# Performance work log

Measured on AMD Instinct MI355X. Metric: run time of the kernel, lower is better.

The kernel has to match this reference:

```python
import jax, jax.numpy as jnp
import numpy as np

N, L, H, E, V, PAD = 128, 64, 512, 512, 32000, 0


def setup_inputs() -> dict:
    key = jax.random.key(0)
    ks = jax.random.split(key, 8)
    s_in = 1.0 / np.sqrt(E)
    s_sani = 1.0 / np.sqrt(2 * H)
    s_out = 1.0 / np.sqrt(H)
    labels = jax.random.randint(ks[0], (N, L), 0, V)
    emb_table = jax.random.normal(ks[1], (V, E), jnp.float32) * 0.02
    emb_table = emb_table.at[PAD].set(0.0)  # padding_idx row is zero-initialized
    W_in = jax.random.uniform(ks[2], (H, E), jnp.float32, -s_in, s_in)
    b_in = jax.random.uniform(ks[3], (H,), jnp.float32, -s_in, s_in)
    W_sani = jax.random.uniform(ks[4], (H, 2 * H), jnp.float32, -s_sani, s_sani)
    b_sani = jax.random.uniform(ks[5], (H,), jnp.float32, -s_sani, s_sani)
    W_out = jax.random.uniform(ks[6], (E, H), jnp.float32, -s_out, s_out)
    b_out = jax.random.uniform(ks[7], (E,), jnp.float32, -s_out, s_out)
    return dict(labels=labels, emb_table=emb_table, W_in=W_in, b_in=b_in,
                W_sani=W_sani, b_sani=b_sani, W_out=W_out, b_out=b_out)


def reference(labels, emb_table, W_in, b_in, W_sani, b_sani, W_out, b_out):
    n, l = labels.shape
    emb = emb_table[labels]                                   # [N,L,E]
    x = jnp.einsum('nle,he->nlh', emb, W_in) + b_in           # [N,L,H] input conversion
    h_dim = W_in.shape[0]

    def step(states, sc):
        s, h0 = sc                                            # h0: [N,H]
        def body(li, carry):
            h, st = carry
            prev = st[li]                                     # hiddenStateLast[li]
            new_h = jnp.concatenate([prev, h], axis=-1) @ W_sani.T + b_sani
            take = li < s                                     # triangular mask
            return (jnp.where(take, new_h, h),
                    st.at[li].set(jnp.where(take, h, prev)))
        h, states = jax.lax.fori_loop(0, l, body, (h0, states))
        states = states.at[s].set(h)                          # hiddenStateLast[s] = h
        return states, h                                      # outputStates[s] = h

    states0 = jnp.zeros((l, n, h_dim), x.dtype)
    _, outs = jax.lax.scan(step, states0, (jnp.arange(l), jnp.swapaxes(x, 0, 1)))
    # torch: pt.concat(outputStates, dim=0) -> [L*N, H], outputLayer, reshape(N,L,E)
    y = outs.reshape(l * n, h_dim) @ W_out.T + b_out
    y = y.reshape(n, l, E)  # faithful to the original (sequence-major) reshape
    # CrossEntropyLoss with float (probability) targets: classes along dim 1 (L)
    logp = jax.nn.log_softmax(y, axis=1)
    loss = -(emb * logp).sum(axis=1).mean()
    return loss
```

## Files before the change

### kernel.cpp

```cpp
#include <hip/hip_runtime.h>
#include <hip/hip_bf16.h>

typedef __attribute__((ext_vector_type(8))) short short8;
typedef __attribute__((ext_vector_type(4))) float floatx4;

#define NB 128
#define LS 64
#define HD 512
#define ED 512
#define NH 65536
#define LDA 72
#define LDC 136
#define LDCF 132

#define OFF_WIN    0ull
#define OFF_WOUT   524288ull
#define OFF_XT     1048576ull
#define OFF_LVL0   9437184ull
#define OFF_LVL1   17825792ull
#define OFF_OUTS   26214400ull
#define OFF_PHA    34603008ull
#define OFF_PLA    37224448ull
#define OFF_PHB    39845888ull
#define OFF_PLB    42467328ull
#define OFF_BCAT   45088768ull
#define OFF_BETA   52428800ull
#define OFF_PART   52436992ull
#define OFF_WSLO   52437504ull
#define OFF_Y      OFF_LVL0

static __device__ __forceinline__ unsigned short f2b(float f) {
  unsigned u = __float_as_uint(f);
  u += 0x7fffu + ((u >> 16) & 1u);
  return (unsigned short)(u >> 16);
}
static __device__ __forceinline__ float b2f(unsigned short h) {
  return __uint_as_float(((unsigned)h) << 16);
}

static __device__ __forceinline__ void gl_lds16(const unsigned short* g, unsigned short* l) {
  __builtin_amdgcn_global_load_lds(
      (const __attribute__((address_space(1))) void*)g,
      (__attribute__((address_space(3))) void*)l, 16, 0, 0);
}

static __device__ __forceinline__ uint4 cvt8hi(const float* s) {
  floatx4 f0 = *(const floatx4*)s;
  floatx4 f1 = *(const floatx4*)(s + 4);
  float f[8] = {f0.x, f0.y, f0.z, f0.w, f1.x, f1.y, f1.z, f1.w};
  unsigned short b[8];
#pragma unroll
  for (int k = 0; k < 8; ++k) b[k] = f2b(f[k]);
  uint4 u;
  u.x = b[0] | ((unsigned)b[1] << 16); u.y = b[2] | ((unsigned)b[3] << 16);
  u.z = b[4] | ((unsigned)b[5] << 16); u.w = b[6] | ((unsigned)b[7] << 16);
  return u;
}

__device__ __forceinline__ void gemm_core24(const unsigned short* As, const unsigned short* Bs,
                                            floatx4 acc[2][4], int wm, int wn, int lane) {
  const int rb = lane & 15;
  const int kg = (lane >> 4) * 8;
#pragma unroll
  for (int kk = 0; kk < 64; kk += 32) {
    short8 a[2], b[4];
#pragma unroll
    for (int i = 0; i < 2; ++i)
      a[i] = *(const short8*)&As[(wm * 32 + i * 16 + rb) * LDA + kk + kg];
#pragma unroll
    for (int j = 0; j < 4; ++j)
      b[j] = *(const short8*)&Bs[(wn * 64 + j * 16 + rb) * LDA + kk + kg];
#pragma unroll
    for (int i = 0; i < 2; ++i)
#pragma unroll
      for (int j = 0; j < 4; ++j)
        acc[i][j] = __builtin_amdgcn_mfma_f32_16x16x32_bf16(a[i], b[j], acc[i][j], 0, 0, 0);
  }
}

__device__ __forceinline__ void gemm_core64s(const unsigned short* As, const unsigned short* Bs,
                                             floatx4 acc[2][4], int wm, int wn, int lane) {
  const int rb = lane & 15;
  const int kg = (lane >> 4) * 8;
  const int xv = (rb & 7) * 8;
#pragma unroll
  for (int kk = 0; kk < 64; kk += 32) {
    const int co = (kk + kg) ^ xv;
    short8 a[2], b[4];
#pragma unroll
    for (int i = 0; i < 2; ++i)
      a[i] = *(const short8*)&As[(wm * 32 + i * 16 + rb) * 64 + co];
#pragma unroll
    for (int j = 0; j < 4; ++j)
      b[j] = *(const short8*)&Bs[(wn * 64 + j * 16 + rb) * 64 + co];
#pragma unroll
    for (int i = 0; i < 2; ++i)
#pragma unroll
      for (int j = 0; j < 4; ++j)
        acc[i][j] = __builtin_amdgcn_mfma_f32_16x16x32_bf16(a[i], b[j], acc[i][j], 0, 0, 0);
  }
}

__device__ __forceinline__ void stageA_emb(unsigned short* As, const float* table,
                                           const int* labels, int m0, int k0, int tid) {
  int r = tid >> 3, kc = (tid & 7) * 8;
#pragma unroll
  for (int p = 0; p < 2; ++p) {
    int row = r + p * 32;
    const float* s = table + (size_t)labels[m0 + row] * ED + k0 + kc;
    *(uint4*)&As[row * LDA + kc] = cvt8hi(s);
  }
}

__device__ __forceinline__ void stageB(unsigned short* Bs, const unsigned short* src, int ldB, int tid) {
  int r = tid >> 3, kc = (tid & 7) * 8;
#pragma unroll
  for (int p = 0; p < 4; ++p)
    *(uint4*)&Bs[(r + p * 32) * LDA + kc] = *(const uint4*)(src + (size_t)(r + p * 32) * ldB + kc);
}

__global__ __launch_bounds__(256) void k_gemm_emb(const float* __restrict__ table,
                                                  const int* __restrict__ labels,
                                                  const unsigned short* __restrict__ Wb,
                                                  const float* __restrict__ bias,
                                                  unsigned short* __restrict__ xt,
                                                  unsigned short* __restrict__ outs) {
  __shared__ unsigned short As[64 * LDA];
  __shared__ unsigned short Bs[128 * LDA];
  int tid = threadIdx.x;
  int mtile = blockIdx.x >> 2, ntile = blockIdx.x & 3;
  int m0 = mtile * 64, n0 = ntile * 128;
  int lane = tid & 63, wave = tid >> 6, wm = wave >> 1, wn = wave & 1;
  floatx4 acc[2][4] = {};
  for (int k0 = 0; k0 < 512; k0 += 64) {
    stageA_emb(As, table, labels, m0, k0, tid);
    stageB(Bs, Wb + (size_t)n0 * 512 + k0, 512, tid);
    __syncthreads();
    gemm_core24(As, Bs, acc, wm, wn, lane);
    __syncthreads();
  }
  int rb = lane & 15, rg = (lane >> 4) * 4;
#pragma unroll
  for (int i = 0; i < 2; ++i)
#pragma unroll
    for (int j = 0; j < 4; ++j) {
      int col = n0 + wn * 64 + j * 16 + rb;
      float bv = bias[col];
#pragma unroll
      for (int reg = 0; reg < 4; ++reg) {
        int m = m0 + wm * 32 + i * 16 + rg + reg;
        int n = m >> 6, l = m & 63;
        unsigned short v = f2b(acc[i][j][reg] + bv);
        xt[((size_t)l * NB + n) * HD + col] = v;
        if (l == 0) outs[(size_t)n * HD + col] = v;
      }
    }
}

__global__ __launch_bounds__(256) void k_cvtw(const float* __restrict__ Win,
                                              const float* __restrict__ Wsani,
                                              const float* __restrict__ Wout,
                                              unsigned short* __restrict__ dWin,
                                              unsigned short* __restrict__ dBcat1,
                                              unsigned short* __restrict__ dWsLo,
                                              unsigned short* __restrict__ dWout) {
  int i = blockIdx.x * 256 + threadIdx.x;
  if (i < 65536 || i >= 196608) {
    const float* src = (i < 65536) ? Win : Wout;
    unsigned short* dst = (i < 65536) ? dWin : dWout;
    int off = (i < 65536) ? i : i - 196608;
    floatx4 v = *(const floatx4*)(src + (size_t)off * 4);
    uint2 u;
    u.x = (unsigned)f2b(v.x) | ((unsigned)f2b(v.y) << 16);
    u.y = (unsigned)f2b(v.z) | ((unsigned)f2b(v.w) << 16);
    *(uint2*)(dst + (size_t)off * 4) = u;
  } else {
    int off = i - 65536;
    floatx4 v = *(const floatx4*)(Wsani + (size_t)off * 4);
    float f[4] = {v.x, v.y, v.z, v.w};
    unsigned short hb[4], lb[4];
#pragma unroll
    for (int k = 0; k < 4; ++k) {
      hb[k] = f2b(f[k]);
      lb[k] = f2b(f[k] - b2f(hb[k]));
    }
    uint2 h, l;
    h.x = hb[0] | ((unsigned)hb[1] << 16); h.y = hb[2] | ((unsigned)hb[3] << 16);
    l.x = lb[0] | ((unsigned)lb[1] << 16); l.y = lb[2] | ((unsigned)lb[3] << 16);
    *(uint2*)(dBcat1 + (size_t)off * 4) = h;
    *(uint2*)(dWsLo + (size_t)off * 4) = l;
  }
}

__global__ __launch_bounds__(256) void k_trW(const float* __restrict__ Ws,
                                             unsigned short* __restrict__ Phi,
                                             unsigned short* __restrict__ Plo) {
  __shared__ float t[64][65];
  int mat = blockIdx.x >> 6, tile = blockIdx.x & 63;
  int a0 = (tile >> 3) * 64, b0 = (tile & 7) * 64;
  int coloff = (mat == 0) ? 512 : 0;
  for (int pp = 0; pp < 16; ++pp) {
    int idx = pp * 256 + threadIdx.x, rr = idx >> 6, cc = idx & 63;
    t[rr][cc] = Ws[(size_t)(b0 + rr) * 1024 + coloff + a0 + cc];
  }
  __syncthreads();
  for (int pp = 0; pp < 16; ++pp) {
    int idx = pp * 256 + threadIdx.x, rr = idx >> 6, cc = idx & 63;
    float f = t[cc][rr];
    unsigned short hi = f2b(f);
    size_t o = (size_t)mat * 262144 + (size_t)(a0 + rr) * 512 + b0 + cc;
    Phi[o] = hi;
    Plo[o] = f2b(f - b2f(hi));
  }
}

__global__ __launch_bounds__(256) void k_coef(const unsigned short* __restrict__ Phi,
                                              const unsigned short* __restrict__ Plo,
                                              unsigned short* __restrict__ PhiOut,
                                              unsigned short* __restrict__ PloOut,
                                              const unsigned short* __restrict__ WsHi,
                                              const unsigned short* __restrict__ WsLo,
                                              int m) {
  __shared__ unsigned short lds[24576];
  unsigned short* const A0 = lds;
  unsigned short* const A1 = lds + 4096;
  unsigned short* const B0 = lds + 8192;
  unsigned short* const B1 = lds + 16384;
  const int tid = threadIdx.x;
  const int j = blockIdx.x >> 5, tile = blockIdx.x & 31;
  const int k0r = (tile >> 2) * 64, n0 = (tile & 3) * 128;
  const int lane = tid & 63, wave = tid >> 6, wm = wave >> 1, wn = wave & 1;
  const int rr_ = tid >> 3;
  const int kcs = (((tid & 7) ^ ((tid >> 3) & 7))) * 8;
  const int t_first = (j <= m) ? 0 : 1;
  const int nterms = ((j <= m) ? 1 : 0) + ((j >= 1) ? 1 : 0);
  const int nsteps = nterms * 24;

  floatx4 acc[2][4] = {};

#define STAGE_C(Ab, Bb, u)                                                           \
  { int term_ = t_first + (((u) >= 24) ? 1 : 0);                                     \
    int v_ = ((u) >> 3) % 3;                                                         \
    int t0_ = ((u) & 7) * 64;                                                        \
    const unsigned short* As_ = ((v_ == 2) ? Plo : Phi)                              \
        + (size_t)(term_ ? (j - 1) : j) * 262144 + (size_t)k0r * 512 + t0_;          \
    const unsigned short* Bs_ = ((v_ == 1) ? WsLo : WsHi)                            \
        + (size_t)n0 * 1024 + (term_ ? 0 : 512) + t0_;                               \
    unsigned short* lA = (Ab) + (tid >> 6) * 512;                                    \
    unsigned short* lB = (Bb) + (tid >> 6) * 512;                                    \
    gl_lds16(As_ + (size_t)rr_ * 512 + kcs, lA);                                     \
    gl_lds16(As_ + (size_t)(rr_ + 32) * 512 + kcs, lA + 2048);                       \
    gl_lds16(Bs_ + (size_t)rr_ * 1024 + kcs, lB);                                    \
    gl_lds16(Bs_ + (size_t)(rr_ + 32) * 1024 + kcs, lB + 2048);                      \
    gl_lds16(Bs_ + (size_t)(rr_ + 64) * 1024 + kcs, lB + 4096);                      \
    gl_lds16(Bs_ + (size_t)(rr_ + 96) * 1024 + kcs, lB + 6144); }

  STAGE_C(A0, B0, 0)
  __syncthreads();
  for (int u = 0; u < nsteps; u += 2) {
    if (u + 1 < nsteps) STAGE_C(A1, B1, u + 1)
    gemm_core64s(A0, B0, acc, wm, wn, lane);
    __syncthreads();
    if (u + 2 < nsteps) STAGE_C(A0, B0, u + 2)
    gemm_core64s(A1, B1, acc, wm, wn, lane);
    __syncthreads();
  }
#undef STAGE_C

  const int rb = lane & 15, rg = (lane >> 4) * 4;
#pragma unroll
  for (int i = 0; i < 2; ++i)
#pragma unroll
    for (int jj = 0; jj < 4; ++jj) {
      int col = n0 + wn * 64 + jj * 16 + rb;
#pragma unroll
      for (int reg = 0; reg < 4; ++reg) {
        int row = wm * 32 + i * 16 + rg + reg;
        float f = acc[i][jj][reg];
        unsigned short hi = f2b(f);
        size_t o = (size_t)j * 262144 + (size_t)(k0r + row) * 512 + col;
        PhiOut[o] = hi;
        PloOut[o] = f2b(f - b2f(hi));
      }
    }
}

__global__ __launch_bounds__(256) void k_trB(const unsigned short* __restrict__ Phi,
                                             unsigned short* __restrict__ Bout,
                                             int r) {
  __shared__ unsigned short t[64][68];
  int q = blockIdx.x >> 6, tile = blockIdx.x & 63;
  int t0 = (tile >> 3) * 64, i0 = (tile & 7) * 64;
  const unsigned short* P = Phi + (size_t)(r - q) * 262144;
  int ldB = (r + 1) * 512;
  for (int pp = 0; pp < 16; ++pp) {
    int idx = pp * 256 + threadIdx.x, rr = idx >> 6, cc = idx & 63;
    t[rr][cc] = P[(size_t)(t0 + rr) * 512 + i0 + cc];
  }
  __syncthreads();
  for (int pp = 0; pp < 16; ++pp) {
    int idx = pp * 256 + threadIdx.x, rr = idx >> 6, cc = idx & 63;
    Bout[(size_t)(i0 + rr) * ldB + q * 512 + t0 + cc] = t[cc][rr];
  }
}

__global__ __launch_bounds__(64) void k_bias_step(const float* __restrict__ Ws,
                                                  const float* __restrict__ b,
                                                  const float* __restrict__ bprev,
                                                  float* __restrict__ bout) {
  int i = blockIdx.x, t = threadIdx.x;
  float p = 0.f;
  for (int k = t; k < 512; k += 64)
    p += (Ws[(size_t)i * 1024 + k] + Ws[(size_t)i * 1024 + 512 + k]) * bprev[k];
#pragma unroll
  for (int off = 32; off > 0; off >>= 1) p += __shfl_down(p, off, 64);
  if (t == 0) bout[i] = p + b[i];
}

__global__ __launch_bounds__(256) void k_step(const unsigned short* __restrict__ src,
                                              unsigned short* __restrict__ dst,
                                              unsigned short* __restrict__ outs,
                                              const unsigned short* __restrict__ Bcat,
                                              const float* __restrict__ beta,
                                              int L_prev, int m, int nmain, int g) {
  __shared__ unsigned short lds[24576];
  unsigned short* const A0 = lds;
  unsigned short* const A1 = lds + 4096;
  unsigned short* const B0 = lds + 8192;
  unsigned short* const B1 = lds + 16384;
  const int tid = threadIdx.x, bid = blockIdx.x;
  const int mainWG = 32 * g;
  int r, s, nb0, n0;
  if (bid < mainWG) {
    const int xcd = bid & 7, w = bid >> 3;
    const int sgrp = xcd >> 1, ngrp = xcd & 1;
    const int s_rel = sgrp * g + (w >> 2);
    if (s_rel >= nmain) return;
    const int sub2 = w & 3;
    nb0 = (sub2 >> 1) * 64;
    n0 = (ngrp * 2 + (sub2 & 1)) * 128;
    r = m; s = L_prev + m + s_rel;
  } else {
    const int db = bid - mainWG;
    r = 1 + (db >> 3);
    const int sub = db & 7;
    nb0 = (sub >> 2) * 64; n0 = (sub & 3) * 128;
    s = L_prev + r;
  }
  const int ldB = (r + 1) * 512;
  const unsigned short* Bp = Bcat + (size_t)262144 * (((r - 1) * (r + 2)) >> 1);
  const unsigned short* abase = src + (size_t)(s - r) * NH + (size_t)nb0 * HD;
  const float* bet = beta + (size_t)(r - 1) * 512;
  const int nk = (r + 1) * 8;
  const int lane = tid & 63, wave = tid >> 6, wm = wave >> 1, wn = wave & 1;
  const int rr_ = tid >> 3;
  const int kcs = (((tid & 7) ^ ((tid >> 3) & 7))) * 8;

  floatx4 acc[2][4] = {};

#define STAGE(Ab, Bb, kcol)                                                          \
  { int q_ = (kcol) >> 9, ac_ = (kcol) & 511;                                        \
    const unsigned short* a0_ = abase + (size_t)q_ * NH + ac_;                       \
    unsigned short* lA = (Ab) + (tid >> 6) * 512;                                    \
    unsigned short* lB = (Bb) + (tid >> 6) * 512;                                    \
    gl_lds16(a0_ + (size_t)rr_ * HD + kcs, lA);                                      \
    gl_lds16(a0_ + (size_t)(rr_ + 32) * HD + kcs, lA + 2048);                        \
    gl_lds16(Bp + (size_t)(n0 + rr_) * ldB + (kcol) + kcs, lB);                      \
    gl_lds16(Bp + (size_t)(n0 + rr_ + 32) * ldB + (kcol) + kcs, lB + 2048);          \
    gl_lds16(Bp + (size_t)(n0 + rr_ + 64) * ldB + (kcol) + kcs, lB + 4096);          \
    gl_lds16(Bp + (size_t)(n0 + rr_ + 96) * ldB + (kcol) + kcs, lB + 6144); }

  STAGE(A0, B0, 0)
  __syncthreads();
  for (int k = 0; k < nk; k += 2) {
    if (k + 1 < nk) STAGE(A1, B1, (k + 1) * 64)
    gemm_core64s(A0, B0, acc, wm, wn, lane);
    __syncthreads();
    if (k + 2 < nk) STAGE(A0, B0, (k + 2) * 64)
    gemm_core64s(A1, B1, acc, wm, wn, lane);
    __syncthreads();
  }
#undef STAGE

  unsigned short* Ct = lds;
  const int rbc = lane & 15, rg = (lane >> 4) * 4;
#pragma unroll
  for (int i = 0; i < 2; ++i)
#pragma unroll
    for (int j = 0; j < 4; ++j) {
      int col = wn * 64 + j * 16 + rbc;
      float bv = bet[n0 + col];
#pragma unroll
      for (int reg = 0; reg < 4; ++reg) {
        int row = wm * 32 + i * 16 + rg + reg;
        Ct[row * LDC + col] = f2b(acc[i][j][reg] + bv);
      }
    }
  __syncthreads();
  const bool wdst = (r == m);
  const bool wout = (r < m) || (s == L_prev + m);
  unsigned short* d1 = dst  + (size_t)s * NH + (size_t)nb0 * HD + n0;
  unsigned short* d2 = outs + (size_t)s * NH + (size_t)nb0 * HD + n0;
  const int lrow = tid >> 4, lcol = (tid & 15) * 8;
#pragma unroll
  for (int sweep = 0; sweep < 4; ++sweep) {
    int row = sweep * 16 + lrow;
    uint4 v = *(const uint4*)&Ct[row * LDC + lcol];
    if (wdst) *(uint4*)(d1 + (size_t)row * HD + lcol) = v;
    if (wout) *(uint4*)(d2 + (size_t)row * HD + lcol) = v;
  }
}

__global__ __launch_bounds__(256) void k_gemm_out(const unsigned short* __restrict__ outs,
                                                  const unsigned short* __restrict__ Wb,
                                                  const float* __restrict__ bias,
                                                  float* __restrict__ Y) {
  __shared__ unsigned short lds[24576];
  unsigned short* const A0 = lds;
  unsigned short* const A1 = lds + 4096;
  unsigned short* const B0 = lds + 8192;
  unsigned short* const B1 = lds + 16384;
  const int tid = threadIdx.x;
  const int mtile = blockIdx.x >> 2, ntile = blockIdx.x & 3;
  const int m0 = mtile * 64, n0 = ntile * 128;
  const int lane = tid & 63, wave = tid >> 6, wm = wave >> 1, wn = wave & 1;
  const int rr_ = tid >> 3;
  const int kcs = (((tid & 7) ^ ((tid >> 3) & 7))) * 8;
  const unsigned short* abase = outs + (size_t)m0 * 512;
  const unsigned short* Bp = Wb + (size_t)n0 * 512;

  floatx4 acc[2][4] = {};

#define STAGE_O(Ab, Bb, kcol)                                                        \
  { unsigned short* lA = (Ab) + (tid >> 6) * 512;                                    \
    unsigned short* lB = (Bb) + (tid >> 6) * 512;                                    \
    gl_lds16(abase + (size_t)rr_ * 512 + (kcol) + kcs, lA);                          \
    gl_lds16(abase + (size_t)(rr_ + 32) * 512 + (kcol) + kcs, lA + 2048);            \
    gl_lds16(Bp + (size_t)rr_ * 512 + (kcol) + kcs, lB);                             \
    gl_lds16(Bp + (size_t)(rr_ + 32) * 512 + (kcol) + kcs, lB + 2048);               \
    gl_lds16(Bp + (size_t)(rr_ + 64) * 512 + (kcol) + kcs, lB + 4096);               \
    gl_lds16(Bp + (size_t)(rr_ + 96) * 512 + (kcol) + kcs, lB + 6144); }

  STAGE_O(A0, B0, 0)
  __syncthreads();
  for (int k = 0; k < 8; k += 2) {
    if (k + 1 < 8) STAGE_O(A1, B1, (k + 1) * 64)
    gemm_core64s(A0, B0, acc, wm, wn, lane);
    __syncthreads();
    if (k + 2 < 8) STAGE_O(A0, B0, (k + 2) * 64)
    gemm_core64s(A1, B1, acc, wm, wn, lane);
    __syncthreads();
  }
#undef STAGE_O

  float* Ctf = (float*)lds;
  const int rbc = lane & 15, rg = (lane >> 4) * 4;
#pragma unroll
  for (int i = 0; i < 2; ++i)
#pragma unroll
    for (int j = 0; j < 4; ++j) {
      int col = wn * 64 + j * 16 + rbc;
      float bv = bias[n0 + col];
#pragma unroll
      for (int reg = 0; reg < 4; ++reg) {
        int row = wm * 32 + i * 16 + rg + reg;
        Ctf[row * LDCF + col] = acc[i][j][reg] + bv;
      }
    }
  __syncthreads();
  const int lrow = tid >> 5, lc = (tid & 31) * 4;
#pragma unroll
  for (int sweep = 0; sweep < 8; ++sweep) {
    int row = sweep * 8 + lrow;
    uint4 v = *(const uint4*)&Ctf[row * LDCF + lc];
    *(uint4*)&Y[(size_t)(m0 + row) * 512 + n0 + lc] = v;
  }
}

__global__ void k_copy(const uint4* __restrict__ src, uint4* __restrict__ dst, int n) {
  int i = blockIdx.x * blockDim.x + threadIdx.x;
  if (i < n) dst[i] = src[i];
}

__global__ __launch_bounds__(256) void k_loss(const float* __restrict__ Y,
                                              const float* __restrict__ table,
                                              const int* __restrict__ labels,
                                              float* __restrict__ partials) {
  int n = blockIdx.x, tid = threadIdx.x;
  float total = 0.f;
#pragma unroll
  for (int e2 = 0; e2 < 2; ++e2) {
    int e = e2 * 256 + tid;
    float mx = -1e30f;
    for (int l = 0; l < 64; ++l)
      mx = fmaxf(mx, Y[(size_t)(n * 64 + l) * 512 + e]);
    float se = 0.f;
    for (int l = 0; l < 64; ++l)
      se += expf(Y[(size_t)(n * 64 + l) * 512 + e] - mx);
    float lse = mx + logf(se);
    for (int l = 0; l < 64; ++l) {
      float embv = table[(size_t)labels[n * 64 + l] * ED + e];
      total += embv * (Y[(size_t)(n * 64 + l) * 512 + e] - lse);
    }
  }
  __shared__ float red[256];
  red[tid] = total;
  __syncthreads();
  for (int s2 = 128; s2 > 0; s2 >>= 1) {
    if (tid < s2) red[tid] += red[tid + s2];
    __syncthreads();
  }
  if (tid == 0) partials[n] = red[0];
}

__global__ void k_final(const float* __restrict__ partials, float* __restrict__ out) {
  if (threadIdx.x == 0) {
    double s = 0.0;
    for (int i = 0; i < 128; ++i) s += (double)partials[i];
    out[0] = (float)(-s / 65536.0);
  }
}

extern "C" void kernel_launch(void* const* d_in, const int* in_sizes, int n_in,
                              void* d_out, int out_size, void* d_ws, size_t ws_size,
                              hipStream_t stream) {
  const int*   labels = (const int*)d_in[0];
  const float* table  = (const float*)d_in[1];
  const float* W_in   = (const float*)d_in[2];
  const float* b_in   = (const float*)d_in[3];
  const float* W_sani = (const float*)d_in[4];
  const float* b_sani = (const float*)d_in[5];
  const float* W_out  = (const float*)d_in[6];
  const float* b_out  = (const float*)d_in[7];

  char* ws = (char*)d_ws;
  unsigned short* Win_b  = (unsigned short*)(ws + OFF_WIN);
  unsigned short* Wout_b = (unsigned short*)(ws + OFF_WOUT);
  unsigned short* xt     = (unsigned short*)(ws + OFF_XT);
  unsigned short* lvl0   = (unsigned short*)(ws + OFF_LVL0);
  unsigned short* lvl1   = (unsigned short*)(ws + OFF_LVL1);
  unsigned short* outs   = (unsigned short*)(ws + OFF_OUTS);
  unsigned short* PhiA   = (unsigned short*)(ws + OFF_PHA);
  unsigned short* PloA   = (unsigned short*)(ws + OFF_PLA);
  unsigned short* PhiB   = (unsigned short*)(ws + OFF_PHB);
  unsigned short* PloB   = (unsigned short*)(ws + OFF_PLB);
  unsigned short* Bcat   = (unsigned short*)(ws + OFF_BCAT);
  float*          beta   = (float*)(ws + OFF_BETA);
  float*          parts  = (float*)(ws + OFF_PART);
  unsigned short* WsLo   = (unsigned short*)(ws + OFF_WSLO);
  float*          Y      = (float*)(ws + OFF_Y);

  k_cvtw<<<1024, 256, 0, stream>>>(W_in, W_sani, W_out, Win_b, Bcat, WsLo, Wout_b);
  k_gemm_emb<<<512, 256, 0, stream>>>(table, labels, Win_b, b_in, xt, outs);

  k_copy<<<1, 128, 0, stream>>>((const uint4*)b_sani, (uint4*)beta, 128);
  k_bias_step<<<512, 64, 0, stream>>>(W_sani, b_sani, beta,        beta + 512);
  k_bias_step<<<512, 64, 0, stream>>>(W_sani, b_sani, beta + 512,  beta + 1024);
  k_bias_step<<<512, 64, 0, stream>>>(W_sani, b_sani, beta + 1024, beta + 1536);

  k_trW <<<128, 256, 0, stream>>>(W_sani, PhiA, PloA);
  k_coef<<< 96, 256, 0, stream>>>(PhiA, PloA, PhiB, PloB, Bcat, WsLo, 1);
  k_trB <<<192, 256, 0, stream>>>(PhiB, Bcat + 524288, 2);
  k_coef<<<128, 256, 0, stream>>>(PhiB, PloB, PhiA, PloA, Bcat, WsLo, 2);
  k_trB <<<256, 256, 0, stream>>>(PhiA, Bcat + 1310720, 3);
  k_coef<<<160, 256, 0, stream>>>(PhiA, PloA, PhiB, PloB, Bcat, WsLo, 3);
  k_trB <<<320, 256, 0, stream>>>(PhiB, Bcat + 2359296, 4);

  const unsigned short* srcp = xt;
  for (int j = 1; j <= 16; ++j) {
    int L_prev = 4 * (j - 1);
    int m = (j == 16) ? 3 : 4;
    int nmain = 64 - (L_prev + m);
    int g = (nmain + 3) >> 2;
    unsigned short* dstp = ((j - 1) & 1) ? lvl1 : lvl0;
    k_step<<<32 * g + (m - 1) * 8, 256, 0, stream>>>(srcp, dstp, outs, Bcat, beta,
                                                     L_prev, m, nmain, g);
    srcp = dstp;
  }

  k_gemm_out<<<512, 256, 0, stream>>>(outs, Wout_b, b_out, Y);
  k_loss<<<128, 256, 0, stream>>>(Y, table, labels, parts);
  k_final<<<1, 64, 0, stream>>>(parts, (float*)d_out);
}
```

Baseline: 583.7 us.

## Fuse bias recurrence and B transpose into coef kernels, fold bias copy

Removes the separate k_copy, k_bias_step and k_trB launches. The bias copy moves into an extra block of k_cvtw. Each bias step runs as extra blocks of the matching k_coef launch, and the coef output tile is transposed through LDS and written straight into the Bcat layout. This cuts about seven small kernel launches and one global read-back of the coefficient matrices from the setup chain, at the cost of more register and LDS pressure and a more complex coef kernel.

After: 566.0 us. 1.03x faster.

```diff
diff --git a/kernel.cpp b/kernel.cpp
--- a/kernel.cpp
+++ b/kernel.cpp
@@ -163,7 +163,15 @@
                                               unsigned short* __restrict__ dWin,
                                               unsigned short* __restrict__ dBcat1,
                                               unsigned short* __restrict__ dWsLo,
-                                              unsigned short* __restrict__ dWout) {
+                                              unsigned short* __restrict__ dWout,
+                                              const float* __restrict__ bsani,
+                                              float* __restrict__ beta) {
+  if (blockIdx.x == 1024) {
+    int t = threadIdx.x;
+    beta[t] = bsani[t];
+    beta[t + 256] = bsani[t + 256];
+    return;
+  }
   int i = blockIdx.x * 256 + threadIdx.x;
   if (i < 65536 || i >= 196608) {
     const float* src = (i < 65536) ? Win : Wout;
@@ -220,7 +228,26 @@
                                               unsigned short* __restrict__ PloOut,
                                               const unsigned short* __restrict__ WsHi,
                                               const unsigned short* __restrict__ WsLo,
-                                              int m) {
+                                              int m,
+                                              unsigned short* __restrict__ BcatOut,
+                                              const float* __restrict__ WsF,
+                                              const float* __restrict__ bF,
+                                              const float* __restrict__ bprev,
+                                              float* __restrict__ bout) {
+  const int ngemm = (m + 2) * 32;
+  if ((int)blockIdx.x >= ngemm) {
+    const int bb = blockIdx.x - ngemm;
+    const int w = threadIdx.x >> 6, lane2 = threadIdx.x & 63;
+    const int i = bb * 4 + w;
+    float p = 0.f;
+    for (int k = lane2; k < 512; k += 64)
+      p += (WsF[(size_t)i * 1024 + k] + WsF[(size_t)i * 1024 + 512 + k]) * bprev[k];
+#pragma unroll
+    for (int off = 32; off > 0; off >>= 1) p += __shfl_down(p, off, 64);
+    if (lane2 == 0) bout[i] = p + bF[i];
+    return;
+  }
+
   __shared__ unsigned short lds[24576];
   unsigned short* const A0 = lds;
   unsigned short* const A1 = lds + 4096;
@@ -267,12 +294,14 @@
   }
 #undef STAGE_C
 
+  unsigned short* CtT = lds;
   const int rb = lane & 15, rg = (lane >> 4) * 4;
 #pragma unroll
   for (int i = 0; i < 2; ++i)
 #pragma unroll
     for (int jj = 0; jj < 4; ++jj) {
-      int col = n0 + wn * 64 + jj * 16 + rb;
+      int colL = wn * 64 + jj * 16 + rb;
+      int col = n0 + colL;
 #pragma unroll
       for (int reg = 0; reg < 4; ++reg) {
         int row = wm * 32 + i * 16 + rg + reg;
@@ -281,40 +310,19 @@
         size_t o = (size_t)j * 262144 + (size_t)(k0r + row) * 512 + col;
         PhiOut[o] = hi;
         PloOut[o] = f2b(f - b2f(hi));
+        CtT[colL * 72 + row] = hi;
       }
     }
-}
-
-__global__ __launch_bounds__(256) void k_trB(const unsigned short* __restrict__ Phi,
-                                             unsigned short* __restrict__ Bout,
-                                             int r) {
-  __shared__ unsigned short t[64][68];
-  int q = blockIdx.x >> 6, tile = blockIdx.x & 63;
-  int t0 = (tile >> 3) * 64, i0 = (tile & 7) * 64;
-  const unsigned short* P = Phi + (size_t)(r - q) * 262144;
-  int ldB = (r + 1) * 512;
-  for (int pp = 0; pp < 16; ++pp) {
-    int idx = pp * 256 + threadIdx.x, rr = idx >> 6, cc = idx & 63;
-    t[rr][cc] = P[(size_t)(t0 + rr) * 512 + i0 + cc];
-  }
-  __syncthreads();
-  for (int pp = 0; pp < 16; ++pp) {
-    int idx = pp * 256 + threadIdx.x, rr = idx >> 6, cc = idx & 63;
-    Bout[(size_t)(i0 + rr) * ldB + q * 512 + t0 + cc] = t[cc][rr];
-  }
-}
-
-__global__ __launch_bounds__(64) void k_bias_step(const float* __restrict__ Ws,
-                                                  const float* __restrict__ b,
-                                                  const float* __restrict__ bprev,
-                                                  float* __restrict__ bout) {
-  int i = blockIdx.x, t = threadIdx.x;
-  float p = 0.f;
-  for (int k = t; k < 512; k += 64)
-    p += (Ws[(size_t)i * 1024 + k] + Ws[(size_t)i * 1024 + 512 + k]) * bprev[k];
-#pragma unroll
-  for (int off = 32; off > 0; off >>= 1) p += __shfl_down(p, off, 64);
-  if (t == 0) bout[i] = p + b[i];
+  __syncthreads();
+  const int rr2 = m + 1;
+  const int ldB2 = (rr2 + 1) * 512;
+  const int q = rr2 - j;
+  const int rowi = tid >> 1, half = tid & 1;
+  unsigned short* dB = BcatOut + (size_t)(n0 + rowi) * ldB2 + q * 512 + k0r + half * 32;
+  const unsigned short* sB = &CtT[rowi * 72 + half * 32];
+#pragma unroll
+  for (int c = 0; c < 4; ++c)
+    *(uint4*)(dB + c * 8) = *(const uint4*)(sB + c * 8);
 }
 
 __global__ __launch_bounds__(256) void k_step(const unsigned short* __restrict__ src,
@@ -477,11 +485,6 @@
   }
 }
 
-__global__ void k_copy(const uint4* __restrict__ src, uint4* __restrict__ dst, int n) {
-  int i = blockIdx.x * blockDim.x + threadIdx.x;
-  if (i < n) dst[i] = src[i];
-}
-
 __global__ __launch_bounds__(256) void k_loss(const float* __restrict__ Y,
                                               const float* __restrict__ table,
                                               const int* __restrict__ labels,
@@ -550,21 +553,20 @@
   unsigned short* WsLo   = (unsigned short*)(ws + OFF_WSLO);
   float*          Y      = (float*)(ws + OFF_Y);
 
-  k_cvtw<<<1024, 256, 0, stream>>>(W_in, W_sani, W_out, Win_b, Bcat, WsLo, Wout_b);
+  k_cvtw<<<1025, 256, 0, stream>>>(W_in, W_sani, W_out, Win_b, Bcat, WsLo, Wout_b,
+                                   b_sani, beta);
   k_gemm_emb<<<512, 256, 0, stream>>>(table, labels, Win_b, b_in, xt, outs);
 
-  k_copy<<<1, 128, 0, stream>>>((const uint4*)b_sani, (uint4*)beta, 128);
-  k_bias_step<<<512, 64, 0, stream>>>(W_sani, b_sani, beta,        beta + 512);
-  k_bias_step<<<512, 64, 0, stream>>>(W_sani, b_sani, beta + 512,  beta + 1024);
-  k_bias_step<<<512, 64, 0, stream>>>(W_sani, b_sani, beta + 1024, beta + 1536);
-
-  k_trW <<<128, 256, 0, stream>>>(W_sani, PhiA, PloA);
-  k_coef<<< 96, 256, 0, stream>>>(PhiA, PloA, PhiB, PloB, Bcat, WsLo, 1);
-  k_trB <<<192, 256, 0, stream>>>(PhiB, Bcat + 524288, 2);
-  k_coef<<<128, 256, 0, stream>>>(PhiB, PloB, PhiA, PloA, Bcat, WsLo, 2);
-  k_trB <<<256, 256, 0, stream>>>(PhiA, Bcat + 1310720, 3);
-  k_coef<<<160, 256, 0, stream>>>(PhiA, PloA, PhiB, PloB, Bcat, WsLo, 3);
-  k_trB <<<320, 256, 0, stream>>>(PhiB, Bcat + 2359296, 4);
+  k_trW<<<128, 256, 0, stream>>>(W_sani, PhiA, PloA);
+  k_coef<<< 96 + 128, 256, 0, stream>>>(PhiA, PloA, PhiB, PloB, Bcat, WsLo, 1,
+                                        Bcat + 524288, W_sani, b_sani,
+                                        beta, beta + 512);
+  k_coef<<<128 + 128, 256, 0, stream>>>(PhiB, PloB, PhiA, PloA, Bcat, WsLo, 2,
+                                        Bcat + 1310720, W_sani, b_sani,
+                                        beta + 512, beta + 1024);
+  k_coef<<<160 + 128, 256, 0, stream>>>(PhiA, PloA, PhiB, PloB, Bcat, WsLo, 3,
+                                        Bcat + 2359296, W_sani, b_sani,
+                                        beta + 1024, beta + 1536);
 
   const unsigned short* srcp = xt;
   for (int j = 1; j <= 16; ++j) {
```
